# Optimization experiments

Measured on AMD Instinct MI355X. Metric: run time of the kernel, lower is better.

Reference implementation:

```python
import jax, jax.numpy as jnp
import numpy as np

PI = 3.14159265359  # TFPI constant from the source


def expected_relu(mu, sigma_sq):
    # Expected ReLU of N(mu, sigma_sq); exact ReLU where sigma_sq == 0 (observed).
    missing = sigma_sq != 0.0
    imputed = jnp.where(missing, sigma_sq, 1e-20)
    s = jnp.sqrt(imputed)
    w = mu / s
    vals = s * (jnp.exp(-0.5 * w * w) / jnp.sqrt(2.0 * PI)
                + 0.5 * w * (1.0 + jax.scipy.special.erf(w / jnp.sqrt(2.0))))
    return jnp.where(missing, vals, 0.5 * (mu + jnp.abs(mu)))


def setup_inputs() -> dict:
    key = jax.random.key(0)
    k0, k1, k2, k3, k4 = jax.random.split(key, 5)
    N, P, C, U = 65536, 256, 3, 512
    x = jax.random.normal(k0, (N, P), dtype=jnp.float32)
    nan_mask = jax.random.bernoulli(k1, 0.15, (N, P))
    x = jnp.where(nan_mask, jnp.nan, x)
    component_means = 0.5 * jax.random.normal(k2, (P, C), dtype=jnp.float32)
    component_vars = jax.random.uniform(k3, (P, C), dtype=jnp.float32, minval=0.5, maxval=1.5)
    component_logits = jnp.ones((C,), dtype=jnp.float32)
    kernel = jax.random.normal(k4, (P, U), dtype=jnp.float32) / np.float32(np.sqrt(P))
    bias = jnp.zeros((U,), dtype=jnp.float32)
    return {"x": x, "component_means": component_means, "component_vars": component_vars,
            "component_logits": component_logits, "kernel": kernel, "bias": bias}


def reference(x, component_means, component_vars, component_logits, kernel, bias):
    # x: [N, P] with NaNs; component_means/vars: [P, C]; logits: [C]; kernel: [P, U]; bias: [U]
    nan_mask = jnp.isnan(x)                       # [N, P]
    x_safe = jnp.where(nan_mask, 0.0, x)          # NaN-free copy (masked out below)
    mu_t = component_means.T                      # [C, P]
    var_t = component_vars.T                      # [C, P]
    # mvn_loglikelihood with NaN entries contributing 0
    q = -jnp.square(x_safe[:, None, :] - mu_t) / var_t / 2.0 - jnp.log(2.0 * PI * var_t) / 2.0  # [N, C, P]
    q = jnp.where(nan_mask[:, None, :], 0.0, q)
    loglik = jnp.sum(q, axis=-1)                  # [N, C]
    reweighted_p = jax.nn.softmax(component_logits + loglik, axis=-1)  # [N, C]
    # Impute missing entries with component means; variance nonzero only where missing
    means = jnp.where(nan_mask[..., None], component_means, x_safe[..., None])   # [N, P, C]
    variances = jnp.where(nan_mask[..., None], component_vars, 0.0)              # [N, P, C]
    layer_mean = jnp.einsum('npc,pu->cnu', means, kernel) + bias                 # [C, N, U]
    layer_var = jnp.einsum('npc,pu->cnu', variances, jnp.square(kernel))         # [C, N, U]
    layer_activation = expected_relu(layer_mean, layer_var)                      # [C, N, U]
    return jnp.einsum('nc,cnu->nu', reweighted_p, layer_activation)              # [N, U]
```

## Files before the change

kernel.cpp:

```cpp
#include <hip/hip_runtime.h>
#include <hip/hip_bf16.h>
#include <math.h>

#define N_ROWS 65536
#define P_DIM  256
#define C_DIM  3
#define U_DIM  512
#define NPLANES 7

#define BM 128
#define BU 64
#define NUT (U_DIM / BU)

typedef __attribute__((ext_vector_type(8))) short short8;
typedef __attribute__((ext_vector_type(4))) float f32x4;
typedef __attribute__((ext_vector_type(4))) float floatx4;
typedef __attribute__((ext_vector_type(4))) unsigned int uint4v;

static __device__ __forceinline__ unsigned short f2bf(float f) {
    unsigned int u = __builtin_bit_cast(unsigned int, f);
    u += 0x7FFFu + ((u >> 16) & 1u);
    return (unsigned short)(u >> 16);
}

static __device__ __forceinline__ float erl(float m, float v) {
    float r = __builtin_amdgcn_rsqf(fmaxf(v, 1e-20f));
    float w = m * r;
    float s = v * r;
    float g = __expf(-0.5f * w * w) * 0.3989422804014327f;
    float aw = fabsf(w);
    float t = __builtin_amdgcn_rcpf(fmaf(0.2316419f, aw, 1.0f));
    float poly = t * (0.319381530f + t * (-0.356563782f + t * (1.781477937f
               + t * (-1.821255978f + t * 1.330274429f))));
    float Phi_pos = 1.0f - g * poly;
    float phi = (w >= 0.0f) ? Phi_pos : 1.0f - Phi_pos;
    float val = s * g + m * phi;
    return (v > 0.0f) ? val : fmaxf(m, 0.0f);
}

__global__ __launch_bounds__(512) void prep_kernel(
    const float* __restrict__ cmeans, const float* __restrict__ cvars,
    const float* __restrict__ kern, unsigned short* __restrict__ Bf,
    float* __restrict__ qtab)
{
    int tid = blockIdx.x * 512 + threadIdx.x;
    const int TOTAL_B = NPLANES * U_DIM * P_DIM;
    if (tid < TOTAL_B) {
        int e    = tid & 7;
        int lane = (tid >> 3) & 63;
        int rest = tid >> 9;
        int pl   = rest % 7;
        int rk   = rest / 7;
        int ks   = rk & 7;
        int uw   = rk >> 3;
        int wc   = uw & 3;
        int ut   = uw >> 2;
        int u = ut * 64 + wc * 16 + (lane & 15);
        int k = ks * 32 + (lane >> 4) * 8 + e;
        float kv = kern[k * U_DIM + u];
        float val;
        if (pl == 0)      val = kv;
        else if (pl <= 3) val = cmeans[k * C_DIM + (pl - 1)] * kv;
        else              val = cvars[k * C_DIM + (pl - 4)] * (kv * kv);
        Bf[tid] = f2bf(val);
    } else if (tid - TOTAL_B < P_DIM) {
        int p = tid - TOTAL_B;
        float a[3], b[3], d[3];
#pragma unroll
        for (int c = 0; c < 3; ++c) {
            float m = cmeans[p * 3 + c];
            float v = cvars[p * 3 + c];
            float iv = 0.5f / v;
            a[c] = iv;
            b[c] = -2.0f * m * iv;
            d[c] = m * m * iv + 0.5f * logf(2.0f * 3.14159265359f * v);
        }
        float* q = qtab + p * 12;
        q[0] = a[0]; q[1] = a[1]; q[2]  = a[2]; q[3]  = 0.f;
        q[4] = b[0]; q[5] = b[1]; q[6]  = b[2]; q[7]  = 0.f;
        q[8] = d[0]; q[9] = d[1]; q[10] = d[2]; q[11] = 0.f;
    }
}

#define LOADB(dst, ksi) do {                                                  \
    _Pragma("unroll")                                                         \
    for (int pl = 0; pl < NPLANES; ++pl)                                      \
        dst[pl] = *(const short8*)(bpw + ((ksi) * 7 + pl) * 512);             \
} while (0)

#define STEP(breg, ksi) do {                                                  \
    __builtin_amdgcn_s_setprio(1);                                            \
    _Pragma("unroll")                                                         \
    for (int r = 0; r < 2; ++r) {                                             \
        short8 a0 = *(const short8*)&xs[aBase + r * 4096 + (ksi) * 512];      \
        short8 a1 = *(const short8*)&mk[aBase + r * 4096 + (ksi) * 512];      \
        acc[0][r] = __builtin_amdgcn_mfma_f32_16x16x32_bf16(a0, breg[0], acc[0][r], 0, 0, 0); \
        _Pragma("unroll")                                                     \
        for (int pl = 1; pl < NPLANES; ++pl)                                  \
            acc[pl][r] = __builtin_amdgcn_mfma_f32_16x16x32_bf16(a1, breg[pl], acc[pl][r], 0, 0, 0); \
    }                                                                         \
    __builtin_amdgcn_s_setprio(0);                                            \
} while (0)

__global__ __launch_bounds__(1024, 4) void main_kernel(
    const float* __restrict__ X, const unsigned short* __restrict__ Bf,
    const float* __restrict__ qtab, const float* __restrict__ logits,
    const float* __restrict__ bias, float* __restrict__ out)
{
    __shared__ unsigned short xs[BM * P_DIM];
    __shared__ unsigned short mk[BM * P_DIM];
    __shared__ float pws[BM][3];

    const int tid = threadIdx.x;
    const int n0 = blockIdx.x * BM;
    const int lane = tid & 63;
    const int wid  = tid >> 6;
    const int l15  = lane & 15;
    const int lk   = lane >> 4;

    {
        const int rowblk = wid >> 1;
        const int ksh    = (wid & 1) * 4;
        const float* Xb = X + (size_t)(n0 + rowblk * 16 + l15) * P_DIM + lk * 8;
        const int ebase = rowblk * 4096 + lk * 128 + l15 * 8;
#pragma unroll
        for (int j = 0; j < 4; ++j) {
            int ks = ksh + j;
            floatx4 v0 = *(const floatx4*)(Xb + ks * 32);
            floatx4 v1 = *(const floatx4*)(Xb + ks * 32 + 4);
            unsigned int wx[4], wm[4];
#pragma unroll
            for (int h = 0; h < 2; ++h) {
                floatx4 v = h ? v1 : v0;
#pragma unroll
                for (int e = 0; e < 2; ++e) {
                    float f0 = v[2 * e], f1 = v[2 * e + 1];
                    bool na0 = !(f0 == f0), na1 = !(f1 == f1);
                    unsigned int s0 = na0 ? 0u : (unsigned int)f2bf(f0);
                    unsigned int s1 = na1 ? 0u : (unsigned int)f2bf(f1);
                    unsigned int m0 = na0 ? 0x3F80u : 0u;
                    unsigned int m1 = na1 ? 0x3F80u : 0u;
                    wx[h * 2 + e] = s0 | (s1 << 16);
                    wm[h * 2 + e] = m0 | (m1 << 16);
                }
            }
            uint4v px = {wx[0], wx[1], wx[2], wx[3]};
            uint4v pm = {wm[0], wm[1], wm[2], wm[3]};
            *(uint4v*)&xs[ebase + ks * 512] = px;
            *(uint4v*)&mk[ebase + ks * 512] = pm;
        }
    }

    {
        int row = tid >> 3;
        int sub = tid & 7;
        const floatx4* xr = (const floatx4*)(X + (size_t)(n0 + row) * P_DIM);
        const floatx4* qt = (const floatx4*)qtab;
        float a0 = 0.f, a1 = 0.f, a2 = 0.f;
#pragma unroll
        for (int i = 0; i < 8; ++i) {
            floatx4 v = xr[sub * 8 + i];
#pragma unroll
            for (int e = 0; e < 4; ++e) {
                float x = v[e];
                int p = sub * 32 + i * 4 + e;
                bool valid = (x == x);
                float xv = valid ? x : 0.f;
                floatx4 qa = qt[p * 3 + 0];
                floatx4 qb = qt[p * 3 + 1];
                floatx4 qd = qt[p * 3 + 2];
                float q0 = fmaf(fmaf(qa[0], xv, qb[0]), xv, qd[0]);
                float q1 = fmaf(fmaf(qa[1], xv, qb[1]), xv, qd[1]);
                float q2 = fmaf(fmaf(qa[2], xv, qb[2]), xv, qd[2]);
                a0 += valid ? q0 : 0.f;
                a1 += valid ? q1 : 0.f;
                a2 += valid ? q2 : 0.f;
            }
        }
#pragma unroll
        for (int off = 1; off < 8; off <<= 1) {
            a0 += __shfl_xor(a0, off);
            a1 += __shfl_xor(a1, off);
            a2 += __shfl_xor(a2, off);
        }
        if (sub == 0) {
            float z0 = logits[0] - a0;
            float z1 = logits[1] - a1;
            float z2 = logits[2] - a2;
            float mx = fmaxf(z0, fmaxf(z1, z2));
            float e0 = __expf(z0 - mx), e1 = __expf(z1 - mx), e2 = __expf(z2 - mx);
            float inv = __builtin_amdgcn_rcpf(e0 + e1 + e2);
            pws[row][0] = e0 * inv;
            pws[row][1] = e1 * inv;
            pws[row][2] = e2 * inv;
        }
    }
    __syncthreads();

    const int wr   = wid >> 2;
    const int wc   = wid & 3;
    const int aBase = wr * 8192 + lk * 128 + l15 * 8;
    const int phase = wc << 1;

#pragma unroll 1
    for (int ut0 = 0; ut0 < NUT; ++ut0) {
        const int ut = (ut0 + phase) & (NUT - 1);
        const unsigned short* bpw = Bf + ((size_t)(ut * 4 + wc) * (8 * 7 * 512)) + (size_t)lane * 8;

        f32x4 acc[NPLANES][2];
#pragma unroll
        for (int pl = 0; pl < NPLANES; ++pl)
#pragma unroll
            for (int r = 0; r < 2; ++r)
                acc[pl][r] = (f32x4){0.f, 0.f, 0.f, 0.f};

        short8 bR[NPLANES];
#pragma unroll 1
        for (int ks = 0; ks < 8; ++ks) {
            LOADB(bR, ks);
            __builtin_amdgcn_sched_barrier(0);
            STEP(bR, ks);
        }

        const int ucol = ut * BU + wc * 16 + l15;
        const float bias_u = bias[ucol];
#pragma unroll
        for (int r = 0; r < 2; ++r) {
            int rloc = wr * 32 + r * 16 + 4 * lk;
#pragma unroll
            for (int q = 0; q < 4; ++q) {
                int rl = rloc + q;
                float p0 = pws[rl][0], p1 = pws[rl][1], p2 = pws[rl][2];
                float y0 = acc[0][r][q] + bias_u;
                float res = p0 * erl(y0 + acc[1][r][q], acc[4][r][q])
                          + p1 * erl(y0 + acc[2][r][q], acc[5][r][q])
                          + p2 * erl(y0 + acc[3][r][q], acc[6][r][q]);
                out[(size_t)(n0 + rl) * U_DIM + ucol] = res;
            }
        }
    }
}

extern "C" void kernel_launch(void* const* d_in, const int* in_sizes, int n_in,
                              void* d_out, int out_size, void* d_ws, size_t ws_size,
                              hipStream_t stream)
{
    const float* X      = (const float*)d_in[0];
    const float* cmeans = (const float*)d_in[1];
    const float* cvars  = (const float*)d_in[2];
    const float* logits = (const float*)d_in[3];
    const float* kern   = (const float*)d_in[4];
    const float* bias   = (const float*)d_in[5];
    float* out = (float*)d_out;

    char* wsb = (char*)d_ws;
    unsigned short* Bf = (unsigned short*)wsb;
    float* qtab = (float*)(wsb + 1835008);

    hipLaunchKernelGGL(prep_kernel, dim3(1794), dim3(512), 0, stream,
                       cmeans, cvars, kern, Bf, qtab);
    hipLaunchKernelGGL(main_kernel, dim3(N_ROWS / BM), dim3(1024), 0, stream,
                       X, Bf, qtab, logits, bias, out);
}
```

Measured before the change: 272.2 us.

## Fold component-mean imputation into A operand, cutting MFMA count per step

```diff
diff --git a/kernel.cpp b/kernel.cpp
--- a/kernel.cpp
+++ b/kernel.cpp
@@ -6,11 +6,12 @@
 #define P_DIM  256
 #define C_DIM  3
 #define U_DIM  512
-#define NPLANES 7
-
-#define BM 128
-#define BU 64
+
+#define BM 64
+#define BU 128
 #define NUT (U_DIM / BU)
+#define NPL 4
+#define NACC 6
 
 typedef __attribute__((ext_vector_type(8))) short short8;
 typedef __attribute__((ext_vector_type(4))) float f32x4;
@@ -44,24 +45,19 @@
     float* __restrict__ qtab)
 {
     int tid = blockIdx.x * 512 + threadIdx.x;
-    const int TOTAL_B = NPLANES * U_DIM * P_DIM;
+    const int TOTAL_B = NUT * 8 * 8 * NPL * 64 * 8;
     if (tid < TOTAL_B) {
         int e    = tid & 7;
         int lane = (tid >> 3) & 63;
         int rest = tid >> 9;
-        int pl   = rest % 7;
-        int rk   = rest / 7;
-        int ks   = rk & 7;
-        int uw   = rk >> 3;
-        int wc   = uw & 3;
-        int ut   = uw >> 2;
-        int u = ut * 64 + wc * 16 + (lane & 15);
+        int pl   = rest & 3;
+        int ks   = (rest >> 2) & 7;
+        int wc   = (rest >> 5) & 7;
+        int ut   = rest >> 8;
+        int u = ut * BU + wc * 16 + (lane & 15);
         int k = ks * 32 + (lane >> 4) * 8 + e;
         float kv = kern[k * U_DIM + u];
-        float val;
-        if (pl == 0)      val = kv;
-        else if (pl <= 3) val = cmeans[k * C_DIM + (pl - 1)] * kv;
-        else              val = cvars[k * C_DIM + (pl - 4)] * (kv * kv);
+        float val = (pl == 0) ? kv : cvars[k * C_DIM + (pl - 1)] * (kv * kv);
         Bf[tid] = f2bf(val);
     } else if (tid - TOTAL_B < P_DIM) {
         int p = tid - TOTAL_B;
@@ -84,31 +80,39 @@
 
 #define LOADB(dst, ksi) do {                                                  \
     _Pragma("unroll")                                                         \
-    for (int pl = 0; pl < NPLANES; ++pl)                                      \
-        dst[pl] = *(const short8*)(bpw + ((ksi) * 7 + pl) * 512);             \
+    for (int pl = 0; pl < NPL; ++pl)                                          \
+        dst[pl] = *(const short8*)(bpw + ((ksi) * NPL + pl) * 512);           \
 } while (0)
 
 #define STEP(breg, ksi) do {                                                  \
     __builtin_amdgcn_s_setprio(1);                                            \
     _Pragma("unroll")                                                         \
     for (int r = 0; r < 2; ++r) {                                             \
-        short8 a0 = *(const short8*)&xs[aBase + r * 4096 + (ksi) * 512];      \
-        short8 a1 = *(const short8*)&mk[aBase + r * 4096 + (ksi) * 512];      \
-        acc[0][r] = __builtin_amdgcn_mfma_f32_16x16x32_bf16(a0, breg[0], acc[0][r], 0, 0, 0); \
-        _Pragma("unroll")                                                     \
-        for (int pl = 1; pl < NPLANES; ++pl)                                  \
-            acc[pl][r] = __builtin_amdgcn_mfma_f32_16x16x32_bf16(a1, breg[pl], acc[pl][r], 0, 0, 0); \
+        int _ao = aBase + r * 4096 + (ksi) * 512;                             \
+        short8 a1 = *(const short8*)&lA1[_ao];                                \
+        short8 a2 = *(const short8*)&lA2[_ao];                                \
+        short8 a3 = *(const short8*)&lA3[_ao];                                \
+        short8 am = *(const short8*)&lMK[_ao];                                \
+        acc[0][r] = __builtin_amdgcn_mfma_f32_16x16x32_bf16(a1, breg[0], acc[0][r], 0, 0, 0); \
+        acc[1][r] = __builtin_amdgcn_mfma_f32_16x16x32_bf16(a2, breg[0], acc[1][r], 0, 0, 0); \
+        acc[2][r] = __builtin_amdgcn_mfma_f32_16x16x32_bf16(a3, breg[0], acc[2][r], 0, 0, 0); \
+        acc[3][r] = __builtin_amdgcn_mfma_f32_16x16x32_bf16(am, breg[1], acc[3][r], 0, 0, 0); \
+        acc[4][r] = __builtin_amdgcn_mfma_f32_16x16x32_bf16(am, breg[2], acc[4][r], 0, 0, 0); \
+        acc[5][r] = __builtin_amdgcn_mfma_f32_16x16x32_bf16(am, breg[3], acc[5][r], 0, 0, 0); \
     }                                                                         \
     __builtin_amdgcn_s_setprio(0);                                            \
 } while (0)
 
 __global__ __launch_bounds__(1024, 4) void main_kernel(
     const float* __restrict__ X, const unsigned short* __restrict__ Bf,
-    const float* __restrict__ qtab, const float* __restrict__ logits,
-    const float* __restrict__ bias, float* __restrict__ out)
+    const float* __restrict__ cmeans, const float* __restrict__ qtab,
+    const float* __restrict__ logits, const float* __restrict__ bias,
+    float* __restrict__ out)
 {
-    __shared__ unsigned short xs[BM * P_DIM];
-    __shared__ unsigned short mk[BM * P_DIM];
+    __shared__ unsigned short lA1[BM * P_DIM];
+    __shared__ unsigned short lA2[BM * P_DIM];
+    __shared__ unsigned short lA3[BM * P_DIM];
+    __shared__ unsigned short lMK[BM * P_DIM];
     __shared__ float pws[BM][3];
 
     const int tid = threadIdx.x;
@@ -119,51 +123,64 @@
     const int lk   = lane >> 4;
 
     {
-        const int rowblk = wid >> 1;
-        const int ksh    = (wid & 1) * 4;
+        const int rowblk = wid >> 2;
         const float* Xb = X + (size_t)(n0 + rowblk * 16 + l15) * P_DIM + lk * 8;
         const int ebase = rowblk * 4096 + lk * 128 + l15 * 8;
 #pragma unroll
-        for (int j = 0; j < 4; ++j) {
-            int ks = ksh + j;
+        for (int j = 0; j < 2; ++j) {
+            int ks = (wid & 3) * 2 + j;
             floatx4 v0 = *(const floatx4*)(Xb + ks * 32);
             floatx4 v1 = *(const floatx4*)(Xb + ks * 32 + 4);
-            unsigned int wx[4], wm[4];
-#pragma unroll
-            for (int h = 0; h < 2; ++h) {
-                floatx4 v = h ? v1 : v0;
-#pragma unroll
-                for (int e = 0; e < 2; ++e) {
-                    float f0 = v[2 * e], f1 = v[2 * e + 1];
-                    bool na0 = !(f0 == f0), na1 = !(f1 == f1);
-                    unsigned int s0 = na0 ? 0u : (unsigned int)f2bf(f0);
-                    unsigned int s1 = na1 ? 0u : (unsigned int)f2bf(f1);
-                    unsigned int m0 = na0 ? 0x3F80u : 0u;
-                    unsigned int m1 = na1 ? 0x3F80u : 0u;
-                    wx[h * 2 + e] = s0 | (s1 << 16);
-                    wm[h * 2 + e] = m0 | (m1 << 16);
+            const float* mup = cmeans + (size_t)(ks * 32 + lk * 8) * 3;
+            floatx4 mA = *(const floatx4*)(mup);
+            floatx4 mB = *(const floatx4*)(mup + 4);
+            floatx4 mC = *(const floatx4*)(mup + 8);
+            floatx4 mD = *(const floatx4*)(mup + 12);
+            floatx4 mE = *(const floatx4*)(mup + 16);
+            floatx4 mF = *(const floatx4*)(mup + 20);
+            float mu[24];
+#pragma unroll
+            for (int z = 0; z < 4; ++z) {
+                mu[z] = mA[z]; mu[4 + z] = mB[z]; mu[8 + z] = mC[z];
+                mu[12 + z] = mD[z]; mu[16 + z] = mE[z]; mu[20 + z] = mF[z];
+            }
+            unsigned int w1[4], w2[4], w3[4], wm[4];
+#pragma unroll
+            for (int pe = 0; pe < 4; ++pe) {
+#pragma unroll
+                for (int h = 0; h < 2; ++h) {
+                    int e = pe * 2 + h;
+                    float x = (e < 4) ? v0[e] : v1[e - 4];
+                    bool na = !(x == x);
+                    unsigned int b1 = (unsigned int)f2bf(na ? mu[e * 3 + 0] : x);
+                    unsigned int b2 = (unsigned int)f2bf(na ? mu[e * 3 + 1] : x);
+                    unsigned int b3 = (unsigned int)f2bf(na ? mu[e * 3 + 2] : x);
+                    unsigned int bm = na ? 0x3F80u : 0u;
+                    if (h == 0) { w1[pe] = b1; w2[pe] = b2; w3[pe] = b3; wm[pe] = bm; }
+                    else { w1[pe] |= b1 << 16; w2[pe] |= b2 << 16; w3[pe] |= b3 << 16; wm[pe] |= bm << 16; }
                 }
             }
-            uint4v px = {wx[0], wx[1], wx[2], wx[3]};
-            uint4v pm = {wm[0], wm[1], wm[2], wm[3]};
-            *(uint4v*)&xs[ebase + ks * 512] = px;
-            *(uint4v*)&mk[ebase + ks * 512] = pm;
+            int idx = ebase + ks * 512;
+            *(uint4v*)&lA1[idx] = (uint4v){w1[0], w1[1], w1[2], w1[3]};
+            *(uint4v*)&lA2[idx] = (uint4v){w2[0], w2[1], w2[2], w2[3]};
+            *(uint4v*)&lA3[idx] = (uint4v){w3[0], w3[1], w3[2], w3[3]};
+            *(uint4v*)&lMK[idx] = (uint4v){wm[0], wm[1], wm[2], wm[3]};
         }
     }
 
     {
-        int row = tid >> 3;
-        int sub = tid & 7;
+        int row = tid >> 4;
+        int sub = tid & 15;
         const floatx4* xr = (const floatx4*)(X + (size_t)(n0 + row) * P_DIM);
         const floatx4* qt = (const floatx4*)qtab;
         float a0 = 0.f, a1 = 0.f, a2 = 0.f;
 #pragma unroll
-        for (int i = 0; i < 8; ++i) {
-            floatx4 v = xr[sub * 8 + i];
+        for (int i = 0; i < 4; ++i) {
+            floatx4 v = xr[sub * 4 + i];
 #pragma unroll
             for (int e = 0; e < 4; ++e) {
                 float x = v[e];
-                int p = sub * 32 + i * 4 + e;
+                int p = sub * 16 + i * 4 + e;
                 bool valid = (x == x);
                 float xv = valid ? x : 0.f;
                 floatx4 qa = qt[p * 3 + 0];
@@ -178,7 +195,7 @@
             }
         }
 #pragma unroll
-        for (int off = 1; off < 8; off <<= 1) {
+        for (int off = 1; off < 16; off <<= 1) {
             a0 += __shfl_xor(a0, off);
             a1 += __shfl_xor(a1, off);
             a2 += __shfl_xor(a2, off);
@@ -197,29 +214,31 @@
     }
     __syncthreads();
 
-    const int wr   = wid >> 2;
-    const int wc   = wid & 3;
+    const int wr   = wid >> 3;
+    const int wc   = wid & 7;
     const int aBase = wr * 8192 + lk * 128 + l15 * 8;
-    const int phase = wc << 1;
+    const int phase = wc & 3;
 
 #pragma unroll 1
     for (int ut0 = 0; ut0 < NUT; ++ut0) {
         const int ut = (ut0 + phase) & (NUT - 1);
-        const unsigned short* bpw = Bf + ((size_t)(ut * 4 + wc) * (8 * 7 * 512)) + (size_t)lane * 8;
-
-        f32x4 acc[NPLANES][2];
-#pragma unroll
-        for (int pl = 0; pl < NPLANES; ++pl)
+        const unsigned short* bpw = Bf + ((size_t)(ut * 8 + wc) * (8 * NPL * 512)) + (size_t)lane * 8;
+
+        f32x4 acc[NACC][2];
+#pragma unroll
+        for (int pl = 0; pl < NACC; ++pl)
 #pragma unroll
             for (int r = 0; r < 2; ++r)
                 acc[pl][r] = (f32x4){0.f, 0.f, 0.f, 0.f};
 
-        short8 bR[NPLANES];
+        short8 bA[NPL], bB[NPL];
+        LOADB(bA, 0);
 #pragma unroll 1
-        for (int ks = 0; ks < 8; ++ks) {
-            LOADB(bR, ks);
-            __builtin_amdgcn_sched_barrier(0);
-            STEP(bR, ks);
+        for (int ks = 0; ks < 8; ks += 2) {
+            LOADB(bB, ks + 1);
+            STEP(bA, ks);
+            if (ks + 2 < 8) LOADB(bA, ks + 2);
+            STEP(bB, ks + 1);
         }
 
         const int ucol = ut * BU + wc * 16 + l15;
@@ -231,10 +250,9 @@
             for (int q = 0; q < 4; ++q) {
                 int rl = rloc + q;
                 float p0 = pws[rl][0], p1 = pws[rl][1], p2 = pws[rl][2];
-                float y0 = acc[0][r][q] + bias_u;
-                float res = p0 * erl(y0 + acc[1][r][q], acc[4][r][q])
-                          + p1 * erl(y0 + acc[2][r][q], acc[5][r][q])
-                          + p2 * erl(y0 + acc[3][r][q], acc[6][r][q]);
+                float res = p0 * erl(acc[0][r][q] + bias_u, acc[3][r][q])
+                          + p1 * erl(acc[1][r][q] + bias_u, acc[4][r][q])
+                          + p2 * erl(acc[2][r][q] + bias_u, acc[5][r][q]);
                 out[(size_t)(n0 + rl) * U_DIM + ucol] = res;
             }
         }
@@ -255,10 +273,10 @@
 
     char* wsb = (char*)d_ws;
     unsigned short* Bf = (unsigned short*)wsb;
-    float* qtab = (float*)(wsb + 1835008);
-
-    hipLaunchKernelGGL(prep_kernel, dim3(1794), dim3(512), 0, stream,
+    float* qtab = (float*)(wsb + 1048576);
+
+    hipLaunchKernelGGL(prep_kernel, dim3(1025), dim3(512), 0, stream,
                        cmeans, cvars, kern, Bf, qtab);
     hipLaunchKernelGGL(main_kernel, dim3(N_ROWS / BM), dim3(1024), 0, stream,
-                       X, Bf, qtab, logits, bias, out);
-}
+                       X, Bf, cmeans, qtab, logits, bias, out);
+}
```

After: 276.9 us. Within noise of the previous version (+1.7%).
